# Kernel optimization log

Hardware: AMD Instinct MI355X
Metric: run time of the kernel (lower is better)

The kernel has to match this reference:

```python
import jax, jax.numpy as jnp
import numpy as np

EPS_NORM = 1e-12   # torch F.normalize eps
EPS_BN = 1e-5      # BatchNorm1d eps
NEG_SLOPE = 0.01   # LeakyReLU default


def _l2_normalize(x, axis):
    # torch F.normalize: x / max(||x||, eps)
    n = jnp.sqrt(jnp.sum(x * x, axis=axis, keepdims=True))
    return x / jnp.maximum(n, EPS_NORM)


def setup_inputs() -> dict:
    key = jax.random.key(0)
    k1, k2, k3, k4, k5, k6, k7 = jax.random.split(key, 7)
    B, C, N, M, OUT = 8, 128, 4096, 4096, 128
    return {
        "input": jax.random.normal(k1, (B, C, N), dtype=jnp.float32),
        "target_g": jax.random.normal(k2, (B, C, M), dtype=jnp.float32),
        "weight": jax.random.normal(k3, (C, OUT), dtype=jnp.float32) * (1.0 / np.sqrt(OUT)),
        "gamma": jax.random.normal(k4, (OUT,), dtype=jnp.float32),
        "beta": jax.random.normal(k5, (OUT,), dtype=jnp.float32),
        "running_mean": jax.random.normal(k6, (OUT,), dtype=jnp.float32),
        "running_var": jax.random.uniform(k7, (OUT,), dtype=jnp.float32, minval=0.5, maxval=1.5),
    }


def reference(input, target_g, weight, gamma, beta, running_mean, running_var):
    # input: [B, C, N], target_g: [B, C, M]
    # cosine-similarity adjacency: [B, M, N]
    tg = _l2_normalize(target_g, axis=1)
    inp_n = _l2_normalize(input, axis=1)
    adj = jnp.einsum('bcm,bcn->bmn', tg, inp_n)
    adj = jax.nn.softmax(adj, axis=-1)
    # aggregate: [B, M, C]
    agg = jnp.einsum('bmn,bcn->bmc', adj, input)
    # project: [B, M, OUT] -> permute to [B, OUT, M]
    out = jnp.einsum('bmc,co->bom', agg, weight)
    # LeakyReLU then BatchNorm1d (eval mode, running stats)
    out = jnp.where(out >= 0, out, NEG_SLOPE * out)
    inv = jax.lax.rsqrt(running_var + EPS_BN)
    out = (out - running_mean[None, :, None]) * (inv * gamma)[None, :, None] + beta[None, :, None]
    return out
```

## Files before the change

kernel.cpp:

```cpp
#include <hip/hip_runtime.h>
#include <hip/hip_bf16.h>

#define BATCH 8
#define CDIM 128
#define NDIM 4096

typedef __bf16 bf16x8 __attribute__((ext_vector_type(8)));
typedef float f32x4 __attribute__((ext_vector_type(4)));

#define QT_OFF 0u
#define KT_OFF 8388608u
#define VB_OFF 16777216u
#define WT_OFF 25165824u
#define SC_OFF (WT_OFF + 32768u)
#define BI_OFF (SC_OFF + 512u)

__device__ __forceinline__ f32x4 mfma16(bf16x8 a, bf16x8 b, f32x4 c) {
    return __builtin_amdgcn_mfma_f32_16x16x32_bf16(a, b, c, 0, 0, 0);
}

__device__ __forceinline__ unsigned pack2bf(float a, float b) {
    unsigned short ul = __builtin_bit_cast(unsigned short, (__bf16)a);
    unsigned short uh = __builtin_bit_cast(unsigned short, (__bf16)b);
    return (unsigned)ul | ((unsigned)uh << 16);
}

__device__ __forceinline__ void glds16(const void* g, void* l) {
    __builtin_amdgcn_global_load_lds((__attribute__((address_space(1))) void*)(void*)g,
                                     (__attribute__((address_space(3))) void*)l, 16, 0, 0);
}

__global__ __launch_bounds__(256) void prep_nt(const float* __restrict__ input,
                                               const float* __restrict__ tg,
                                               void* __restrict__ ws) {
    __shared__ float T[128][68];
    __shared__ float psum[4][64];
    __shared__ float rn[64];
    const int n0 = blockIdx.x * 64;
    const int b  = blockIdx.y;
    const int tid = threadIdx.x;
    const float* src = (blockIdx.z == 0 ? input : tg) + (size_t)b * CDIM * NDIM;

    #pragma unroll
    for (int i = 0; i < 8; ++i) {
        int f = tid + i * 256;
        int c = f >> 4;
        int j4 = f & 15;
        *(float4*)&T[c][j4 * 4] = *(const float4*)(src + (size_t)c * NDIM + n0 + j4 * 4);
    }
    __syncthreads();
    {
        int j = tid & 63, part = tid >> 6;
        float ss = 0.f;
        #pragma unroll 8
        for (int c = part * 32; c < part * 32 + 32; ++c) { float x = T[c][j]; ss += x * x; }
        psum[part][j] = ss;
    }
    __syncthreads();
    if (tid < 64) {
        float s = psum[0][tid] + psum[1][tid] + psum[2][tid] + psum[3][tid];
        rn[tid] = 1.0f / fmaxf(sqrtf(s), 1e-12f);
    }
    __syncthreads();

    if (blockIdx.z == 0) {
        __hip_bfloat16* kt = (__hip_bfloat16*)((char*)ws + KT_OFF) + ((size_t)b * NDIM + n0) * CDIM;
        #pragma unroll
        for (int i = 0; i < 16; ++i) {
            int f = tid + i * 256;
            int j = f >> 6, c2 = f & 63;
            float r = rn[j];
            unsigned pk = pack2bf(T[c2 * 2][j] * r, T[c2 * 2 + 1][j] * r);
            *(unsigned*)((unsigned short*)kt + (size_t)j * CDIM + c2 * 2) = pk;
        }
        __hip_bfloat16* vb = (__hip_bfloat16*)((char*)ws + VB_OFF) + (size_t)b * CDIM * NDIM + n0;
        #pragma unroll
        for (int i = 0; i < 8; ++i) {
            int f = tid + i * 256;
            int c = f >> 4, j4 = f & 15;
            float4 v = *(const float4*)&T[c][j4 * 4];
            uint2 pv; pv.x = pack2bf(v.x, v.y); pv.y = pack2bf(v.z, v.w);
            *(uint2*)((unsigned short*)vb + (size_t)c * NDIM + j4 * 4) = pv;
        }
    } else {
        __hip_bfloat16* qt = (__hip_bfloat16*)((char*)ws + QT_OFF) + ((size_t)b * NDIM + n0) * CDIM;
        #pragma unroll
        for (int i = 0; i < 16; ++i) {
            int f = tid + i * 256;
            int j = f >> 6, c2 = f & 63;
            float r = rn[j];
            unsigned pk = pack2bf(T[c2 * 2][j] * r, T[c2 * 2 + 1][j] * r);
            *(unsigned*)((unsigned short*)qt + (size_t)j * CDIM + c2 * 2) = pk;
        }
    }
}

__global__ __launch_bounds__(256) void prep_w(const float* __restrict__ wgt,
                                              const float* __restrict__ gamma,
                                              const float* __restrict__ beta,
                                              const float* __restrict__ mean,
                                              const float* __restrict__ var,
                                              void* __restrict__ ws) {
    __hip_bfloat16* wT = (__hip_bfloat16*)((char*)ws + WT_OFF);
    float* sc = (float*)((char*)ws + SC_OFF);
    float* bi = (float*)((char*)ws + BI_OFF);
    const int tid = threadIdx.x;
    #pragma unroll
    for (int i = 0; i < 64; ++i) {
        int f = tid + i * 256;
        int c = f >> 7, o = f & 127;
        wT[o * 128 + c] = __hip_bfloat16(wgt[c * 128 + o]);
    }
    if (tid < 128) {
        float inv = rsqrtf(var[tid] + 1e-5f);
        float s = inv * gamma[tid];
        sc[tid] = s;
        bi[tid] = beta[tid] - mean[tid] * s;
    }
}

__global__ __launch_bounds__(512, 4) void flash2(const void* __restrict__ ws_,
                                                 float* __restrict__ out) {
    extern __shared__ char smem[];
    const char* ws = (const char*)ws_;
    const __hip_bfloat16* Qt = (const __hip_bfloat16*)(ws + QT_OFF);
    const __hip_bfloat16* Kt = (const __hip_bfloat16*)(ws + KT_OFF);
    const __hip_bfloat16* Vb = (const __hip_bfloat16*)(ws + VB_OFF);
    const __hip_bfloat16* wT = (const __hip_bfloat16*)(ws + WT_OFF);
    const float* scale = (const float*)(ws + SC_OFF);
    const float* bias  = (const float*)(ws + BI_OFF);

    const int b  = blockIdx.y;
    const int m0 = blockIdx.x * 64;
    const int tid = threadIdx.x;
    const int w = tid >> 6, lane = tid & 63;
    const int h = w >> 2, wq = w & 3;
    const int li = lane & 15, q = lane >> 4;

    char* sK = smem + h * 32768;
    char* sV = smem + h * 32768 + 16384;
    char* sP = smem + 65536 + h * 8192;

    const __hip_bfloat16* kgb = Kt + (size_t)b * NDIM * CDIM;
    const __hip_bfloat16* vgb = Vb + (size_t)b * CDIM * NDIM;

    bf16x8 qf[4];
    {
        const __hip_bfloat16* qrow = Qt + ((size_t)b * NDIM + m0 + wq * 16 + li) * CDIM;
        #pragma unroll
        for (int ks = 0; ks < 4; ++ks)
            qf[ks] = *(const bf16x8*)(qrow + ks * 32 + q * 8);
    }

    const __hip_bfloat16* gK[4]; char* lK[4];
    const __hip_bfloat16* gV[4]; char* lV[4];
    #pragma unroll
    for (int i = 0; i < 4; ++i) {
        int s = (wq * 4 + i) * 64 + lane;
        int n = s >> 4, sl = s & 15;
        int cc = sl ^ (n & 15);
        gK[i] = kgb + (size_t)(h * 2048 + n) * CDIM + cc * 8;
        lK[i] = sK + (wq * 4 + i) * 1024;
        int s2 = s;
        int c = s2 >> 3, sl8 = s2 & 7;
        int nc = sl8 ^ (c & 7);
        gV[i] = vgb + (size_t)c * NDIM + h * 2048 + nc * 8;
        lV[i] = sV + (wq * 4 + i) * 1024;
    }

    const f32x4 z4 = {0.f, 0.f, 0.f, 0.f};
    f32x4 oaccT[2][4];
    #pragma unroll
    for (int ca = 0; ca < 2; ++ca)
        #pragma unroll
        for (int mb = 0; mb < 4; ++mb) oaccT[ca][mb] = z4;
    float lacc = 0.f;

    for (int it = 0; it < 32; ++it) {
        __syncthreads();
        #pragma unroll
        for (int i = 0; i < 4; ++i) { glds16(gK[i], lK[i]); gK[i] += 64 * CDIM; }
        #pragma unroll
        for (int i = 0; i < 4; ++i) { glds16(gV[i], lV[i]); gV[i] += 64; }
        __syncthreads();

        f32x4 st[4];
        #pragma unroll
        for (int nb = 0; nb < 4; ++nb) st[nb] = z4;
        #pragma unroll
        for (int nb = 0; nb < 4; ++nb) {
            #pragma unroll
            for (int ks = 0; ks < 4; ++ks) {
                int n = nb * 16 + li;
                int sl = (ks * 4 + q) ^ li;
                bf16x8 kf = *(const bf16x8*)(sK + n * 256 + sl * 16);
                st[nb] = mfma16(kf, qf[ks], st[nb]);
            }
        }

        #pragma unroll
        for (int nb = 0; nb < 4; ++nb) {
            float p0 = __expf(st[nb][0] - 1.0f);
            float p1 = __expf(st[nb][1] - 1.0f);
            float p2 = __expf(st[nb][2] - 1.0f);
            float p3 = __expf(st[nb][3] - 1.0f);
            lacc += (p0 + p1) + (p2 + p3);
            uint2 pk; pk.x = pack2bf(p0, p1); pk.y = pack2bf(p2, p3);
            int slot8 = (nb * 4 + q) ^ ((li & 7) << 1);
            *(uint2*)(sP + (wq * 16 + li) * 128 + slot8 * 8) = pk;
        }
        __syncthreads();

        #pragma unroll
        for (int ks2 = 0; ks2 < 2; ++ks2) {
            bf16x8 pf[4];
            #pragma unroll
            for (int mb = 0; mb < 4; ++mb) {
                int m = mb * 16 + li;
                int slot8 = ((ks2 * 4 + q) * 2) ^ ((li & 7) << 1);
                pf[mb] = *(const bf16x8*)(sP + m * 128 + slot8 * 8);
            }
            #pragma unroll
            for (int ca = 0; ca < 2; ++ca) {
                int c = (wq * 2 + ca) * 16 + li;
                int sl = (ks2 * 4 + q) ^ (li & 7);
                bf16x8 vf = *(const bf16x8*)(sV + c * 128 + sl * 16);
                #pragma unroll
                for (int mb = 0; mb < 4; ++mb)
                    oaccT[ca][mb] = mfma16(vf, pf[mb], oaccT[ca][mb]);
            }
        }
    }

    float lsum = lacc;
    lsum += __shfl_xor(lsum, 16, 64);
    lsum += __shfl_xor(lsum, 32, 64);

    __syncthreads();
    float* lLds = (float*)(smem + 34304);
    if (q == 0) lLds[h * 64 + wq * 16 + li] = lsum;
    float* sO32 = (float*)smem;
    if (h == 1) {
        #pragma unroll
        for (int ca = 0; ca < 2; ++ca)
            #pragma unroll
            for (int mb = 0; mb < 4; ++mb)
                #pragma unroll
                for (int r = 0; r < 4; ++r)
                    sO32[((wq * 2 + ca) * 16 + q * 4 + r) * 66 + mb * 16 + li] =
                        oaccT[ca][mb][r];
    }
    __syncthreads();
    __hip_bfloat16* sAgg = (__hip_bfloat16*)(smem + 36864);
    if (h == 0) {
        float linv[4];
        #pragma unroll
        for (int mb = 0; mb < 4; ++mb)
            linv[mb] = 1.0f / (lLds[mb * 16 + li] + lLds[64 + mb * 16 + li]);
        #pragma unroll
        for (int ca = 0; ca < 2; ++ca) {
            #pragma unroll
            for (int mb = 0; mb < 4; ++mb) {
                float v0 = (oaccT[ca][mb][0] + sO32[((wq*2+ca)*16 + q*4 + 0) * 66 + mb*16 + li]) * linv[mb];
                float v1 = (oaccT[ca][mb][1] + sO32[((wq*2+ca)*16 + q*4 + 1) * 66 + mb*16 + li]) * linv[mb];
                float v2 = (oaccT[ca][mb][2] + sO32[((wq*2+ca)*16 + q*4 + 2) * 66 + mb*16 + li]) * linv[mb];
                float v3 = (oaccT[ca][mb][3] + sO32[((wq*2+ca)*16 + q*4 + 3) * 66 + mb*16 + li]) * linv[mb];
                uint2 pk; pk.x = pack2bf(v0, v1); pk.y = pack2bf(v2, v3);
                int m = mb * 16 + li;
                int c8 = (wq * 2 + ca) * 4 + q;
                int slot8 = c8 ^ ((m & 7) << 1);
                *(uint2*)((char*)sAgg + m * 256 + slot8 * 8) = pk;
            }
        }
    }
    __syncthreads();

    const int mslice = (w & 3) * 16;
    const int ohalf = (w >> 2) * 64;
    f32x4 racc[4];
    #pragma unroll
    for (int ob = 0; ob < 4; ++ob) racc[ob] = z4;
    #pragma unroll
    for (int ks = 0; ks < 4; ++ks) {
        int slot8 = ((ks * 4 + q) * 2) ^ ((li & 7) << 1);
        bf16x8 af = *(const bf16x8*)((char*)sAgg + (mslice + li) * 256 + slot8 * 8);
        #pragma unroll
        for (int ob = 0; ob < 4; ++ob) {
            bf16x8 wf = *(const bf16x8*)(wT + (size_t)(ohalf + ob * 16 + li) * CDIM + ks * 32 + q * 8);
            racc[ob] = mfma16(af, wf, racc[ob]);
        }
    }

    float* sRes = (float*)smem;
    #pragma unroll
    for (int ob = 0; ob < 4; ++ob) {
        int o = ohalf + ob * 16 + li;
        float sc = scale[o], bi = bias[o];
        #pragma unroll
        for (int r = 0; r < 4; ++r) {
            float v = racc[ob][r];
            v = (v >= 0.0f) ? v : 0.01f * v;
            v = v * sc + bi;
            sRes[o * 68 + mslice + q * 4 + r] = v;
        }
    }
    __syncthreads();

    float* outb = out + (size_t)b * CDIM * NDIM + m0;
    #pragma unroll
    for (int i = 0; i < 4; ++i) {
        int f = tid + i * 512;
        int o = f >> 4, mq = f & 15;
        *(float4*)(outb + (size_t)o * NDIM + mq * 4) = *(const float4*)(sRes + o * 68 + mq * 4);
    }
}

extern "C" void kernel_launch(void* const* d_in, const int* in_sizes, int n_in,
                              void* d_out, int out_size, void* d_ws, size_t ws_size,
                              hipStream_t stream) {
    const float* input  = (const float*)d_in[0];
    const float* tg     = (const float*)d_in[1];
    const float* weight = (const float*)d_in[2];
    const float* gamma  = (const float*)d_in[3];
    const float* beta   = (const float*)d_in[4];
    const float* rmean  = (const float*)d_in[5];
    const float* rvar   = (const float*)d_in[6];
    float* out = (float*)d_out;

    (void)in_sizes; (void)n_in; (void)out_size; (void)ws_size;

    hipFuncSetAttribute(reinterpret_cast<const void*>(flash2),
                        hipFuncAttributeMaxDynamicSharedMemorySize, 81920);

    dim3 gprep(NDIM / 64, BATCH, 2);
    prep_nt<<<gprep, 256, 0, stream>>>(input, tg, d_ws);
    prep_w<<<dim3(1), 256, 0, stream>>>(weight, gamma, beta, rmean, rvar, d_ws);
    dim3 gflash(NDIM / 64, BATCH);
    flash2<<<gflash, 512, 81920, stream>>>(d_ws, out);
}
```

Measured before the change: 201.7 us.

## Retile flash kernel warps as 2x2 M/N sub-blocks and transpose prep staging

```diff
diff --git a/kernel.cpp b/kernel.cpp
--- a/kernel.cpp
+++ b/kernel.cpp
@@ -33,7 +33,7 @@
 __global__ __launch_bounds__(256) void prep_nt(const float* __restrict__ input,
                                                const float* __restrict__ tg,
                                                void* __restrict__ ws) {
-    __shared__ float T[128][68];
+    __shared__ float Tt[64][129];
     __shared__ float psum[4][64];
     __shared__ float rn[64];
     const int n0 = blockIdx.x * 64;
@@ -44,16 +44,19 @@
     #pragma unroll
     for (int i = 0; i < 8; ++i) {
         int f = tid + i * 256;
-        int c = f >> 4;
-        int j4 = f & 15;
-        *(float4*)&T[c][j4 * 4] = *(const float4*)(src + (size_t)c * NDIM + n0 + j4 * 4);
+        int c = f >> 4, j4 = f & 15;
+        float4 v = *(const float4*)(src + (size_t)c * NDIM + n0 + j4 * 4);
+        Tt[j4 * 4 + 0][c] = v.x;
+        Tt[j4 * 4 + 1][c] = v.y;
+        Tt[j4 * 4 + 2][c] = v.z;
+        Tt[j4 * 4 + 3][c] = v.w;
     }
     __syncthreads();
     {
         int j = tid & 63, part = tid >> 6;
         float ss = 0.f;
         #pragma unroll 8
-        for (int c = part * 32; c < part * 32 + 32; ++c) { float x = T[c][j]; ss += x * x; }
+        for (int c = part * 32; c < part * 32 + 32; ++c) { float x = Tt[j][c]; ss += x * x; }
         psum[part][j] = ss;
     }
     __syncthreads();
@@ -63,34 +66,27 @@
     }
     __syncthreads();
 
+    __hip_bfloat16* dstT = (__hip_bfloat16*)((char*)ws + (blockIdx.z == 0 ? KT_OFF : QT_OFF))
+                           + ((size_t)b * NDIM + n0) * CDIM;
+    #pragma unroll
+    for (int i = 0; i < 8; ++i) {
+        int f = tid + i * 256;
+        int j = f >> 5, c4 = f & 31;
+        float r = rn[j];
+        float4 v = *(const float4*)&Tt[j][c4 * 4];
+        uint2 pk; pk.x = pack2bf(v.x * r, v.y * r); pk.y = pack2bf(v.z * r, v.w * r);
+        *(uint2*)((unsigned short*)dstT + (size_t)j * CDIM + c4 * 4) = pk;
+    }
     if (blockIdx.z == 0) {
-        __hip_bfloat16* kt = (__hip_bfloat16*)((char*)ws + KT_OFF) + ((size_t)b * NDIM + n0) * CDIM;
-        #pragma unroll
-        for (int i = 0; i < 16; ++i) {
-            int f = tid + i * 256;
-            int j = f >> 6, c2 = f & 63;
-            float r = rn[j];
-            unsigned pk = pack2bf(T[c2 * 2][j] * r, T[c2 * 2 + 1][j] * r);
-            *(unsigned*)((unsigned short*)kt + (size_t)j * CDIM + c2 * 2) = pk;
-        }
         __hip_bfloat16* vb = (__hip_bfloat16*)((char*)ws + VB_OFF) + (size_t)b * CDIM * NDIM + n0;
         #pragma unroll
         for (int i = 0; i < 8; ++i) {
             int f = tid + i * 256;
             int c = f >> 4, j4 = f & 15;
-            float4 v = *(const float4*)&T[c][j4 * 4];
-            uint2 pv; pv.x = pack2bf(v.x, v.y); pv.y = pack2bf(v.z, v.w);
+            float x0 = Tt[j4 * 4 + 0][c], x1 = Tt[j4 * 4 + 1][c];
+            float x2 = Tt[j4 * 4 + 2][c], x3 = Tt[j4 * 4 + 3][c];
+            uint2 pv; pv.x = pack2bf(x0, x1); pv.y = pack2bf(x2, x3);
             *(uint2*)((unsigned short*)vb + (size_t)c * NDIM + j4 * 4) = pv;
-        }
-    } else {
-        __hip_bfloat16* qt = (__hip_bfloat16*)((char*)ws + QT_OFF) + ((size_t)b * NDIM + n0) * CDIM;
-        #pragma unroll
-        for (int i = 0; i < 16; ++i) {
-            int f = tid + i * 256;
-            int j = f >> 6, c2 = f & 63;
-            float r = rn[j];
-            unsigned pk = pack2bf(T[c2 * 2][j] * r, T[c2 * 2 + 1][j] * r);
-            *(unsigned*)((unsigned short*)qt + (size_t)j * CDIM + c2 * 2) = pk;
         }
     }
 }
@@ -119,7 +115,7 @@
     }
 }
 
-__global__ __launch_bounds__(512, 4) void flash2(const void* __restrict__ ws_,
+__global__ __launch_bounds__(512, 4) void flash3(const void* __restrict__ ws_,
                                                  float* __restrict__ out) {
     extern __shared__ char smem[];
     const char* ws = (const char*)ws_;
@@ -136,139 +132,162 @@
     const int w = tid >> 6, lane = tid & 63;
     const int h = w >> 2, wq = w & 3;
     const int li = lane & 15, q = lane >> 4;
-
-    char* sK = smem + h * 32768;
-    char* sV = smem + h * 32768 + 16384;
-    char* sP = smem + 65536 + h * 8192;
+    const int ns = wq >> 1, ms = wq & 1;
+    const int cs = wq >> 1;
 
     const __hip_bfloat16* kgb = Kt + (size_t)b * NDIM * CDIM;
     const __hip_bfloat16* vgb = Vb + (size_t)b * CDIM * NDIM;
 
-    bf16x8 qf[4];
-    {
-        const __hip_bfloat16* qrow = Qt + ((size_t)b * NDIM + m0 + wq * 16 + li) * CDIM;
+    bf16x8 qf[2][4];
+    #pragma unroll
+    for (int mb = 0; mb < 2; ++mb) {
+        const __hip_bfloat16* qrow = Qt + ((size_t)b * NDIM + m0 + ms * 32 + mb * 16 + li) * CDIM;
         #pragma unroll
         for (int ks = 0; ks < 4; ++ks)
-            qf[ks] = *(const bf16x8*)(qrow + ks * 32 + q * 8);
-    }
-
-    const __hip_bfloat16* gK[4]; char* lK[4];
-    const __hip_bfloat16* gV[4]; char* lV[4];
+            qf[mb][ks] = *(const bf16x8*)(qrow + ks * 32 + q * 8);
+    }
+
+    unsigned kOff[2][4];
+    #pragma unroll
+    for (int nb = 0; nb < 2; ++nb)
+        #pragma unroll
+        for (int ks = 0; ks < 4; ++ks) {
+            int n = ns * 32 + nb * 16 + li;
+            kOff[nb][ks] = h * 32768 + n * 256 + (((ks * 4 + q) ^ li)) * 16;
+        }
+    unsigned vOff[2][4];
+    #pragma unroll
+    for (int k2 = 0; k2 < 2; ++k2)
+        #pragma unroll
+        for (int ca = 0; ca < 4; ++ca) {
+            int c = cs * 64 + ca * 16 + li;
+            vOff[k2][ca] = h * 32768 + 16384 + c * 128 + (((k2 * 4 + q) ^ (li & 7))) * 16;
+        }
+    unsigned pOff[2][2];
+    #pragma unroll
+    for (int k2 = 0; k2 < 2; ++k2)
+        #pragma unroll
+        for (int mb = 0; mb < 2; ++mb)
+            pOff[k2][mb] = 65536 + h * 8192 + (ms * 32 + mb * 16 + li) * 128
+                           + (((k2 * 8 + q * 2) ^ ((li & 7) << 1))) * 8;
+    unsigned wOff[2][2];
+    #pragma unroll
+    for (int nb = 0; nb < 2; ++nb)
+        #pragma unroll
+        for (int mb = 0; mb < 2; ++mb)
+            wOff[nb][mb] = 65536 + h * 8192 + (ms * 32 + mb * 16 + li) * 128
+                           + (((ns * 8 + nb * 4 + q) ^ ((li & 7) << 1))) * 8;
+
+    const __hip_bfloat16* gK[4]; const __hip_bfloat16* gV[4];
+    unsigned lKo[4], lVo[4];
     #pragma unroll
     for (int i = 0; i < 4; ++i) {
         int s = (wq * 4 + i) * 64 + lane;
         int n = s >> 4, sl = s & 15;
         int cc = sl ^ (n & 15);
         gK[i] = kgb + (size_t)(h * 2048 + n) * CDIM + cc * 8;
-        lK[i] = sK + (wq * 4 + i) * 1024;
-        int s2 = s;
-        int c = s2 >> 3, sl8 = s2 & 7;
+        lKo[i] = h * 32768 + (wq * 4 + i) * 1024;
+        int c = s >> 3, sl8 = s & 7;
         int nc = sl8 ^ (c & 7);
         gV[i] = vgb + (size_t)c * NDIM + h * 2048 + nc * 8;
-        lV[i] = sV + (wq * 4 + i) * 1024;
+        lVo[i] = h * 32768 + 16384 + (wq * 4 + i) * 1024;
     }
 
     const f32x4 z4 = {0.f, 0.f, 0.f, 0.f};
-    f32x4 oaccT[2][4];
-    #pragma unroll
-    for (int ca = 0; ca < 2; ++ca)
-        #pragma unroll
-        for (int mb = 0; mb < 4; ++mb) oaccT[ca][mb] = z4;
-    float lacc = 0.f;
+    f32x4 oacc[4][2];
+    #pragma unroll
+    for (int ca = 0; ca < 4; ++ca) { oacc[ca][0] = z4; oacc[ca][1] = z4; }
+    float lac0 = 0.f, lac1 = 0.f;
 
     for (int it = 0; it < 32; ++it) {
         __syncthreads();
         #pragma unroll
-        for (int i = 0; i < 4; ++i) { glds16(gK[i], lK[i]); gK[i] += 64 * CDIM; }
-        #pragma unroll
-        for (int i = 0; i < 4; ++i) { glds16(gV[i], lV[i]); gV[i] += 64; }
+        for (int i = 0; i < 4; ++i) { glds16(gK[i], smem + lKo[i]); gK[i] += 64 * CDIM; }
+        #pragma unroll
+        for (int i = 0; i < 4; ++i) { glds16(gV[i], smem + lVo[i]); gV[i] += 64; }
         __syncthreads();
 
-        f32x4 st[4];
-        #pragma unroll
-        for (int nb = 0; nb < 4; ++nb) st[nb] = z4;
-        #pragma unroll
-        for (int nb = 0; nb < 4; ++nb) {
+        #pragma unroll
+        for (int nb = 0; nb < 2; ++nb) {
+            f32x4 st0 = z4, st1 = z4;
             #pragma unroll
             for (int ks = 0; ks < 4; ++ks) {
-                int n = nb * 16 + li;
-                int sl = (ks * 4 + q) ^ li;
-                bf16x8 kf = *(const bf16x8*)(sK + n * 256 + sl * 16);
-                st[nb] = mfma16(kf, qf[ks], st[nb]);
-            }
-        }
-
-        #pragma unroll
-        for (int nb = 0; nb < 4; ++nb) {
-            float p0 = __expf(st[nb][0] - 1.0f);
-            float p1 = __expf(st[nb][1] - 1.0f);
-            float p2 = __expf(st[nb][2] - 1.0f);
-            float p3 = __expf(st[nb][3] - 1.0f);
-            lacc += (p0 + p1) + (p2 + p3);
-            uint2 pk; pk.x = pack2bf(p0, p1); pk.y = pack2bf(p2, p3);
-            int slot8 = (nb * 4 + q) ^ ((li & 7) << 1);
-            *(uint2*)(sP + (wq * 16 + li) * 128 + slot8 * 8) = pk;
+                bf16x8 kf = *(const bf16x8*)(smem + kOff[nb][ks]);
+                st0 = mfma16(kf, qf[0][ks], st0);
+                st1 = mfma16(kf, qf[1][ks], st1);
+            }
+            {
+                float p0 = __expf(st0[0] - 1.0f), p1 = __expf(st0[1] - 1.0f);
+                float p2 = __expf(st0[2] - 1.0f), p3 = __expf(st0[3] - 1.0f);
+                lac0 += (p0 + p1) + (p2 + p3);
+                uint2 pk; pk.x = pack2bf(p0, p1); pk.y = pack2bf(p2, p3);
+                *(uint2*)(smem + wOff[nb][0]) = pk;
+            }
+            {
+                float p0 = __expf(st1[0] - 1.0f), p1 = __expf(st1[1] - 1.0f);
+                float p2 = __expf(st1[2] - 1.0f), p3 = __expf(st1[3] - 1.0f);
+                lac1 += (p0 + p1) + (p2 + p3);
+                uint2 pk; pk.x = pack2bf(p0, p1); pk.y = pack2bf(p2, p3);
+                *(uint2*)(smem + wOff[nb][1]) = pk;
+            }
         }
         __syncthreads();
 
         #pragma unroll
-        for (int ks2 = 0; ks2 < 2; ++ks2) {
-            bf16x8 pf[4];
+        for (int k2 = 0; k2 < 2; ++k2) {
+            bf16x8 pf0 = *(const bf16x8*)(smem + pOff[k2][0]);
+            bf16x8 pf1 = *(const bf16x8*)(smem + pOff[k2][1]);
             #pragma unroll
-            for (int mb = 0; mb < 4; ++mb) {
-                int m = mb * 16 + li;
-                int slot8 = ((ks2 * 4 + q) * 2) ^ ((li & 7) << 1);
-                pf[mb] = *(const bf16x8*)(sP + m * 128 + slot8 * 8);
-            }
-            #pragma unroll
-            for (int ca = 0; ca < 2; ++ca) {
-                int c = (wq * 2 + ca) * 16 + li;
-                int sl = (ks2 * 4 + q) ^ (li & 7);
-                bf16x8 vf = *(const bf16x8*)(sV + c * 128 + sl * 16);
-                #pragma unroll
-                for (int mb = 0; mb < 4; ++mb)
-                    oaccT[ca][mb] = mfma16(vf, pf[mb], oaccT[ca][mb]);
-            }
-        }
-    }
-
-    float lsum = lacc;
-    lsum += __shfl_xor(lsum, 16, 64);
-    lsum += __shfl_xor(lsum, 32, 64);
+            for (int ca = 0; ca < 4; ++ca) {
+                bf16x8 vf = *(const bf16x8*)(smem + vOff[k2][ca]);
+                oacc[ca][0] = mfma16(vf, pf0, oacc[ca][0]);
+                oacc[ca][1] = mfma16(vf, pf1, oacc[ca][1]);
+            }
+        }
+    }
+
+    lac0 += __shfl_xor(lac0, 16, 64); lac0 += __shfl_xor(lac0, 32, 64);
+    lac1 += __shfl_xor(lac1, 16, 64); lac1 += __shfl_xor(lac1, 32, 64);
 
     __syncthreads();
     float* lLds = (float*)(smem + 34304);
-    if (q == 0) lLds[h * 64 + wq * 16 + li] = lsum;
+    if (q == 0) {
+        lLds[(h * 2 + ns) * 64 + ms * 32 + li] = lac0;
+        lLds[(h * 2 + ns) * 64 + ms * 32 + 16 + li] = lac1;
+    }
     float* sO32 = (float*)smem;
     if (h == 1) {
         #pragma unroll
-        for (int ca = 0; ca < 2; ++ca)
+        for (int ca = 0; ca < 4; ++ca)
             #pragma unroll
-            for (int mb = 0; mb < 4; ++mb)
+            for (int mb = 0; mb < 2; ++mb)
                 #pragma unroll
                 for (int r = 0; r < 4; ++r)
-                    sO32[((wq * 2 + ca) * 16 + q * 4 + r) * 66 + mb * 16 + li] =
-                        oaccT[ca][mb][r];
+                    sO32[(cs * 64 + ca * 16 + q * 4 + r) * 66 + ms * 32 + mb * 16 + li] =
+                        oacc[ca][mb][r];
     }
     __syncthreads();
     __hip_bfloat16* sAgg = (__hip_bfloat16*)(smem + 36864);
     if (h == 0) {
-        float linv[4];
-        #pragma unroll
-        for (int mb = 0; mb < 4; ++mb)
-            linv[mb] = 1.0f / (lLds[mb * 16 + li] + lLds[64 + mb * 16 + li]);
-        #pragma unroll
-        for (int ca = 0; ca < 2; ++ca) {
+        float linv[2]; int mm[2];
+        #pragma unroll
+        for (int mb = 0; mb < 2; ++mb) {
+            int m = ms * 32 + mb * 16 + li;
+            mm[mb] = m;
+            linv[mb] = 1.0f / (lLds[m] + lLds[64 + m] + lLds[128 + m] + lLds[192 + m]);
+        }
+        #pragma unroll
+        for (int ca = 0; ca < 4; ++ca) {
             #pragma unroll
-            for (int mb = 0; mb < 4; ++mb) {
-                float v0 = (oaccT[ca][mb][0] + sO32[((wq*2+ca)*16 + q*4 + 0) * 66 + mb*16 + li]) * linv[mb];
-                float v1 = (oaccT[ca][mb][1] + sO32[((wq*2+ca)*16 + q*4 + 1) * 66 + mb*16 + li]) * linv[mb];
-                float v2 = (oaccT[ca][mb][2] + sO32[((wq*2+ca)*16 + q*4 + 2) * 66 + mb*16 + li]) * linv[mb];
-                float v3 = (oaccT[ca][mb][3] + sO32[((wq*2+ca)*16 + q*4 + 3) * 66 + mb*16 + li]) * linv[mb];
+            for (int mb = 0; mb < 2; ++mb) {
+                int m = mm[mb];
+                float v0 = (oacc[ca][mb][0] + sO32[(cs*64 + ca*16 + q*4 + 0) * 66 + m]) * linv[mb];
+                float v1 = (oacc[ca][mb][1] + sO32[(cs*64 + ca*16 + q*4 + 1) * 66 + m]) * linv[mb];
+                float v2 = (oacc[ca][mb][2] + sO32[(cs*64 + ca*16 + q*4 + 2) * 66 + m]) * linv[mb];
+                float v3 = (oacc[ca][mb][3] + sO32[(cs*64 + ca*16 + q*4 + 3) * 66 + m]) * linv[mb];
                 uint2 pk; pk.x = pack2bf(v0, v1); pk.y = pack2bf(v2, v3);
-                int m = mb * 16 + li;
-                int c8 = (wq * 2 + ca) * 4 + q;
-                int slot8 = c8 ^ ((m & 7) << 1);
+                int c8 = cs * 16 + ca * 4 + q;
+                int slot8 = c8 ^ ((li & 7) << 1);
                 *(uint2*)((char*)sAgg + m * 256 + slot8 * 8) = pk;
             }
         }
@@ -329,12 +348,12 @@
 
     (void)in_sizes; (void)n_in; (void)out_size; (void)ws_size;
 
-    hipFuncSetAttribute(reinterpret_cast<const void*>(flash2),
+    hipFuncSetAttribute(reinterpret_cast<const void*>(flash3),
                         hipFuncAttributeMaxDynamicSharedMemorySize, 81920);
 
     dim3 gprep(NDIM / 64, BATCH, 2);
     prep_nt<<<gprep, 256, 0, stream>>>(input, tg, d_ws);
     prep_w<<<dim3(1), 256, 0, stream>>>(weight, gamma, beta, rmean, rvar, d_ws);
     dim3 gflash(NDIM / 64, BATCH);
-    flash2<<<gflash, 512, 81920, stream>>>(d_ws, out);
-}
+    flash3<<<gflash, 512, 81920, stream>>>(d_ws, out);
+}
```

New measurement: 199.5 us. Within noise of the previous version (-1.1%).
